# Performance work log

Hardware: AMD Instinct MI355X
Metric: run time of the kernel (lower is better)

## Reference

```python
import jax, jax.numpy as jnp
import numpy as np

N, P, C, K = 1024, 64, 64, 16
C_MID, C_OUT = 128, 128


def setup_inputs() -> dict:
    key = jax.random.key(0)
    k1, k2, k3, k4 = jax.random.split(key, 4)
    x = jax.random.normal(k1, (N, P, C), dtype=jnp.float32)
    mask = jnp.zeros((N, P), dtype=bool)  # True = padded particle
    # Conv2d(2C -> C_MID, 1x1, no bias); Conv2d(C_MID -> C_OUT, 1x1, no bias)
    W1 = jax.random.normal(k2, (C_MID, 2 * C), dtype=jnp.float32) * 0.05
    W2 = jax.random.normal(k3, (C_OUT, C_MID), dtype=jnp.float32) * 0.05
    # Conv1d(C -> C_OUT, kernel 1, no bias) residual path
    Wres = jax.random.normal(k4, (C_OUT, C), dtype=jnp.float32) * 0.05
    return {"x": x, "mask": mask, "W1": W1, "W2": W2, "Wres": Wres}


def reference(x, mask, W1, W2, Wres):
    n, p, c = x.shape
    k = K
    # residual: Conv1d kernel-1 == per-particle matmul  (N,P,C)->(N,P,C_OUT)
    x_res = jnp.einsum('npc,oc->npo', x, Wres)
    # direction = x with padded rows set to +inf (mask all False here)
    direction = jnp.where(mask[..., None], jnp.inf, x)
    # pairwise L2 distance over channel dim: (N,P,P)
    diff = direction[:, :, None, :] - direction[:, None, :, :]
    dist = jnp.sqrt(jnp.sum(diff * diff, axis=-1))
    # smallest K+1 distances, drop self
    _, idx = jax.lax.top_k(-dist, k + 1)
    knn = idx[..., 1:]  # (N,P,K)
    # faithful to torch: gather along the CHANNEL dim with particle indices
    f_center = jnp.broadcast_to(x[:, :, None, :], (n, p, k, c))  # (N,P,K,C)
    f_neighbor = jnp.take_along_axis(f_center, knn[..., None], axis=-1)  # (N,P,K,1)
    feat = jnp.concatenate([f_center, f_center - f_neighbor], axis=-1)  # (N,P,K,2C)
    # 1x1 conv MLP (channels-last layout)
    h = jax.nn.relu(jnp.einsum('npkc,oc->npko', feat, W1))
    h = jax.nn.relu(jnp.einsum('npkc,oc->npko', h, W2))  # (N,P,K,C_OUT)
    # mask neighbors pointing at padded slots, masked mean over K
    n_valid = p - jnp.sum(mask, axis=-1)  # (N,)
    mask_K = knn >= n_valid[:, None, None]  # (N,P,K) bool
    h = jnp.where(mask_K[..., None], 0.0, h)
    denom = (k - jnp.sum(mask_K, axis=-1)).astype(h.dtype)  # (N,P)
    agg = jnp.sum(h, axis=2) / denom[..., None]  # (N,P,C_OUT)
    return jax.nn.relu(agg + x_res)
```

## Files before the change

### kernel.cpp

```cpp
#include <hip/hip_runtime.h>
#include <hip/hip_bf16.h>

typedef __bf16 bf16x8 __attribute__((ext_vector_type(8)));
typedef float  f32x4  __attribute__((ext_vector_type(4)));
typedef float  f32x2  __attribute__((ext_vector_type(2)));
typedef unsigned long long u64;

#define MFMA_BF16 __builtin_amdgcn_mfma_f32_16x16x32_bf16

#define WS_W2P  (1u << 20)
#define WS_WCP  ((1u << 20) + 32768u)
#define WS_SSUM ((1u << 20) + 65536u)

#define K1_XS   0
#define K1_SD   17408
#define K1_SQ   34048
#define K1_LDS  38144

__global__ __launch_bounds__(256, 3)
void knn_kernel(const float* __restrict__ x, const float* __restrict__ W1,
                const float* __restrict__ W2, const float* __restrict__ Wres,
                unsigned* __restrict__ ws)
{
    __shared__ char smem[K1_LDS];
    float*    xs   = (float*)(smem + K1_XS);
    float*    D    = (float*)(smem + K1_SD);
    float*    sd_t = (float*)(smem + K1_SD);
    unsigned* sqp  = (unsigned*)(smem + K1_SQ);

    const int tid = threadIdx.x;
    const int n   = blockIdx.x;
    const float* __restrict__ xn = x + (size_t)n * 4096;

    #pragma unroll
    for (int i = 0; i < 4; ++i) {
        int e4 = tid + 256 * i;
        f32x4 v = *(const f32x4*)(xn + e4 * 4);
        int row = e4 >> 4, col = (e4 & 15) * 4;
        float* dst = xs + row * 68 + col;
        dst[0] = v[0]; dst[1] = v[1]; dst[2] = v[2]; dst[3] = v[3];
    }
    __syncthreads();

    {
#pragma clang fp contract(off)
        const int p = tid >> 2, rb = tid & 3;
        f32x4 xp4[16];
        const f32x4* xprow = (const f32x4*)(xs + p * 68);
        #pragma unroll
        for (int v = 0; v < 16; ++v) xp4[v] = xprow[v];

        const int d0 = (rb - p) & 3;
        #pragma unroll
        for (int t = 0; t < 8; ++t) {
            int delta = (d0 == 0) ? (4 + 4 * t) : (d0 + 4 * t);
            int q = (p + delta) & 63;
            bool doit = !(delta == 32 && p >= 32);
            if (doit) {
                const f32x4* xq4 = (const f32x4*)(xs + q * 68);
                f32x4 e0 = xp4[0] - xq4[0];
                f32x4 e1 = xp4[1] - xq4[1];
                f32x4 rA = e0 * e0;
                f32x4 rB = e1 * e1;
                #pragma unroll
                for (int b = 1; b < 8; ++b) {
                    f32x4 g0 = xp4[2*b]   - xq4[2*b];   rA = rA + g0 * g0;
                    f32x4 g1 = xp4[2*b+1] - xq4[2*b+1]; rB = rB + g1 * g1;
                }
                float d2 = ((rA[0]+rA[1]) + (rA[2]+rA[3])) + ((rB[0]+rB[1]) + (rB[2]+rB[3]));
                D[p * 65 + q] = d2;
                D[q * 65 + p] = d2;
            }
        }
        __syncthreads();

        u64 keys[16];
        #pragma unroll
        for (int i = 0; i < 16; ++i) {
            int q = 4 * i + rb;
            float d2  = D[p * 65 + q];
            float key = sqrtf(d2);
            unsigned kb = __float_as_uint(key);
            if (q == p) kb = 0x7f800000u;
            keys[i] = ((u64)kb << 8) | (unsigned)q;
        }
        __syncthreads();

        #pragma unroll
        for (int pp = 1; pp < 16; pp <<= 1) {
            #pragma unroll
            for (int k = pp; k >= 1; k >>= 1) {
                #pragma unroll
                for (int j = k & (pp - 1); j + k < 16; j += 2 * k) {
                    #pragma unroll
                    for (int i = 0; i < k; ++i) {
                        if (i + j + k < 16 && ((i + j) / (2 * pp) == (i + j + k) / (2 * pp))) {
                            u64 a = keys[i + j], b = keys[i + j + k];
                            u64 lo = a < b ? a : b;
                            u64 hi = a < b ? b : a;
                            keys[i + j] = lo; keys[i + j + k] = hi;
                        }
                    }
                }
            }
        }
        #pragma unroll
        for (int t = 0; t < 4; ++t) {
            unsigned wq = 0;
            #pragma unroll
            for (int b = 0; b < 4; ++b) {
                int s = 4 * t + b;
                sd_t[(rb * 16 + s) * 65 + p] = __uint_as_float((unsigned)(keys[s] >> 8));
                wq |= ((unsigned)(keys[s] & 0x3fu)) << (8 * b);
            }
            sqp[(rb * 4 + t) * 64 + p] = wq;
        }
    }
    __syncthreads();

    if (tid < 64) {
        const int p = tid;
        float dh[4]; unsigned qh[4]; int ix[4];
        #pragma unroll
        for (int b = 0; b < 4; ++b) {
            ix[b] = 0;
            dh[b] = sd_t[(b * 16) * 65 + p];
            qh[b] = sqp[(b * 4) * 64 + p] & 63u;
        }
        unsigned knacc[4] = {0u, 0u, 0u, 0u};
        for (int s = 0; s < 16; ++s) {
            int bsel = 0; float bd = dh[0]; unsigned bq = qh[0];
            #pragma unroll
            for (int b = 1; b < 4; ++b) {
                bool t = (dh[b] < bd) || (dh[b] == bd && qh[b] < bq);
                if (t) { bd = dh[b]; bq = qh[b]; bsel = b; }
            }
            knacc[s >> 2] |= bq << ((s & 3) * 8);
            int ni = ix[bsel] + 1; ix[bsel] = ni;
            int nc = ni < 15 ? ni : 15;
            float nd = sd_t[(bsel * 16 + nc) * 65 + p];
            unsigned nw = sqp[(bsel * 4 + (nc >> 2)) * 64 + p];
            unsigned nq = (nw >> ((nc & 3) * 8)) & 63u;
            if (ni > 15) nd = __builtin_inff();
            dh[bsel] = nd; qh[bsel] = nq;
        }
        *(uint4*)(ws + (size_t)n * 256 + p * 4) =
            make_uint4(knacc[0], knacc[1], knacc[2], knacc[3]);
    }

    if (n < 32) {
        if (tid < 64) {
            const int l = tid, f = n;
            int ntl = f >> 2, kt = f & 3;
            int o = ntl * 16 + (l & 15);
            int c = kt * 32 + (l >> 4) * 8;
            const float* s0 = W2 + o * 128 + c;
            f32x4 a0 = *(const f32x4*)s0, a1 = *(const f32x4*)(s0 + 4);
            bf16x8 fr;
            fr[0]=(__bf16)a0[0]; fr[1]=(__bf16)a0[1]; fr[2]=(__bf16)a0[2]; fr[3]=(__bf16)a0[3];
            fr[4]=(__bf16)a1[0]; fr[5]=(__bf16)a1[1]; fr[6]=(__bf16)a1[2]; fr[7]=(__bf16)a1[3];
            *(bf16x8*)((__bf16*)((char*)ws + WS_W2P) + (size_t)(f * 64 + l) * 8) = fr;
        }
    } else if (n < 64) {
        if (tid < 64) {
            const int l = tid, f = n - 32;
            int wv = f >> 3, rem = f & 7, ntl = rem >> 1, kt = rem & 1;
            int o = wv * 64 + ntl * 16 + (l & 15);
            int c = kt * 32 + (l >> 4) * 8;
            float v[8];
            if (o < 128) {
                const float* s0 = W1 + o * 128 + c;
                f32x4 a0 = *(const f32x4*)s0,      a1 = *(const f32x4*)(s0 + 4);
                f32x4 b0 = *(const f32x4*)(s0+64), b1 = *(const f32x4*)(s0 + 68);
                v[0]=a0[0]+b0[0]; v[1]=a0[1]+b0[1]; v[2]=a0[2]+b0[2]; v[3]=a0[3]+b0[3];
                v[4]=a1[0]+b1[0]; v[5]=a1[1]+b1[1]; v[6]=a1[2]+b1[2]; v[7]=a1[3]+b1[3];
            } else {
                const float* s0 = Wres + (o - 128) * 64 + c;
                f32x4 a0 = *(const f32x4*)s0, a1 = *(const f32x4*)(s0 + 4);
                v[0]=a0[0]; v[1]=a0[1]; v[2]=a0[2]; v[3]=a0[3];
                v[4]=a1[0]; v[5]=a1[1]; v[6]=a1[2]; v[7]=a1[3];
            }
            bf16x8 fr;
            #pragma unroll
            for (int j = 0; j < 8; ++j) fr[j] = (__bf16)v[j];
            *(bf16x8*)((__bf16*)((char*)ws + WS_WCP) + (size_t)(f * 64 + l) * 8) = fr;
        }
    } else if (n == 64) {
        if (tid < 128) {
            const f32x4* src = (const f32x4*)(W1 + tid * 128 + 64);
            f32x4 a = {0.f, 0.f, 0.f, 0.f};
            #pragma unroll
            for (int i = 0; i < 16; ++i) a += src[i];
            ((float*)((char*)ws + WS_SSUM))[tid] = a[0] + a[1] + a[2] + a[3];
        }
    }
}

#define K2_UB   0
#define K2_XR   32768
#define K2_SS   65536
#define K2_LDS  66048

__global__ __launch_bounds__(256, 2)
void gemm_kernel(const float* __restrict__ x, const unsigned* __restrict__ ws,
                 float* __restrict__ out)
{
    __shared__ char smem[K2_LDS];
    __bf16*   ub   = (__bf16*)(smem + K2_UB);
    __bf16*   xres = (__bf16*)(smem + K2_XR);
    float*    Ssum = (float*)(smem + K2_SS);

    const __bf16* __restrict__ w2p   = (const __bf16*)((const char*)ws + WS_W2P);
    const __bf16* __restrict__ wcp   = (const __bf16*)((const char*)ws + WS_WCP);
    const float*  __restrict__ ssums = (const float*)((const char*)ws + WS_SSUM);

    const int tid  = threadIdx.x;
    const int lane = tid & 63;
    const int w    = tid >> 6;
    const int lm   = lane & 15;
    const int lq   = lane >> 4;
    const int n0   = blockIdx.x * 2;

    if (tid < 128) Ssum[tid] = ssums[tid];

    {
        bf16x8 wcf[4][2];
        #pragma unroll
        for (int ntl = 0; ntl < 4; ++ntl) {
            #pragma unroll
            for (int kt = 0; kt < 2; ++kt)
                wcf[ntl][kt] = *(const bf16x8*)(wcp + (size_t)((w * 8 + ntl * 2 + kt) * 64 + lane) * 8);
        }
        #pragma unroll
        for (int ns = 0; ns < 2; ++ns) {
            const float* xn = x + (size_t)(n0 + ns) * 4096;
            __bf16* ubn = ub   + ns * 8192;
            __bf16* xrn = xres + ns * 8192;
            #pragma unroll
            for (int mt = 0; mt < 4; ++mt) {
                bf16x8 af[2];
                #pragma unroll
                for (int kt = 0; kt < 2; ++kt) {
                    const float* arow = xn + (mt * 16 + lm) * 64 + kt * 32 + lq * 8;
                    f32x4 a0 = *(const f32x4*)arow, a1 = *(const f32x4*)(arow + 4);
                    bf16x8 f;
                    f[0]=(__bf16)a0[0]; f[1]=(__bf16)a0[1]; f[2]=(__bf16)a0[2]; f[3]=(__bf16)a0[3];
                    f[4]=(__bf16)a1[0]; f[5]=(__bf16)a1[1]; f[6]=(__bf16)a1[2]; f[7]=(__bf16)a1[3];
                    af[kt] = f;
                }
                #pragma unroll
                for (int ntl = 0; ntl < 4; ++ntl) {
                    f32x4 acc = {0.f, 0.f, 0.f, 0.f};
                    acc = MFMA_BF16(af[0], wcf[ntl][0], acc, 0, 0, 0);
                    acc = MFMA_BF16(af[1], wcf[ntl][1], acc, 0, 0, 0);
                    int o = w * 64 + ntl * 16 + lm;
                    #pragma unroll
                    for (int r = 0; r < 4; ++r) {
                        int p = mt * 16 + lq * 4 + r;
                        if (o < 128) ubn[p * 128 + o] = (__bf16)acc[r];
                        else         xrn[p * 128 + (o - 128)] = (__bf16)acc[r];
                    }
                }
            }
        }
    }
    __syncthreads();

    {
        bf16x8 w2f[8][4];
        #pragma unroll
        for (int ntl = 0; ntl < 8; ++ntl) {
            #pragma unroll
            for (int kt = 0; kt < 4; ++kt)
                w2f[ntl][kt] = *(const bf16x8*)(w2p + (size_t)((ntl * 4 + kt) * 64 + lane) * 8);
        }
        f32x2 ss2[4][4];
        #pragma unroll
        for (int kt = 0; kt < 4; ++kt) {
            #pragma unroll
            for (int h = 0; h < 4; ++h) {
                ss2[kt][h][0] = Ssum[kt * 32 + lq * 8 + 2 * h];
                ss2[kt][h][1] = Ssum[kt * 32 + lq * 8 + 2 * h + 1];
            }
        }
        const int c0 = lq * 32 + lm;
        const int jsh = (lm & 3) * 8, jwi = lm >> 2;

        #pragma unroll 1
        for (int ns = 0; ns < 2; ++ns) {
            const float*    xn  = x + (size_t)(n0 + ns) * 4096;
            const unsigned* kb  = ws + (size_t)(n0 + ns) * 256;
            const __bf16*   ubn = ub   + ns * 8192;
            const __bf16*   xrn = xres + ns * 8192;
            const size_t outbase = (size_t)(n0 + ns) * 8192;

            unsigned jw_a = kb[w * 4 + jwi];
            unsigned jw_b = kb[(w + 4) * 4 + jwi];
            float sv_next = xn[w * 64 + ((jw_a >> jsh) & 63u)];

            #pragma unroll 1
            for (int pi = 0; pi < 16; ++pi) {
                const int p = w + pi * 4;
                const float sv_p = sv_next;
                jw_a = jw_b;
                if (pi < 15) {
                    if (pi < 14) jw_b = kb[(w + (pi + 2) * 4) * 4 + jwi];
                    sv_next = xn[(p + 4) * 64 + ((jw_a >> jsh) & 63u)];
                }

                const f32x2 sv2 = {sv_p, sv_p};
                f32x4 acc[8];
                #pragma unroll
                for (int ntl = 0; ntl < 8; ++ntl) acc[ntl] = f32x4{0.f, 0.f, 0.f, 0.f};
                #pragma unroll
                for (int kt = 0; kt < 4; ++kt) {
                    bf16x8 upv = *(const bf16x8*)(ubn + p * 128 + kt * 32 + lq * 8);
                    bf16x8 af;
                    #pragma unroll
                    for (int h = 0; h < 4; ++h) {
                        f32x2 u2 = { (float)upv[2*h], (float)upv[2*h+1] };
                        f32x2 m2 = u2 - sv2 * ss2[kt][h];
                        af[2*h]   = (__bf16)fmaxf(m2[0], 0.0f);
                        af[2*h+1] = (__bf16)fmaxf(m2[1], 0.0f);
                    }
                    #pragma unroll
                    for (int ntl = 0; ntl < 8; ++ntl)
                        acc[ntl] = MFMA_BF16(af, w2f[ntl][kt], acc[ntl], 0, 0, 0);
                }
                float part[8];
                #pragma unroll
                for (int ntl = 0; ntl < 8; ++ntl) {
                    part[ntl] = fmaxf(acc[ntl][0], 0.f) + fmaxf(acc[ntl][1], 0.f)
                              + fmaxf(acc[ntl][2], 0.f) + fmaxf(acc[ntl][3], 0.f);
                }
                float s1[4];
                #pragma unroll
                for (int i = 0; i < 4; ++i) {
                    float mine = (lq < 2) ? part[i] : part[4 + i];
                    float thr  = (lq < 2) ? part[4 + i] : part[i];
                    s1[i] = mine + __shfl_xor(thr, 32);
                }
                float r0, r1;
                {
                    float m0 = ((lq & 1) == 0) ? s1[0] : s1[2];
                    float m1 = ((lq & 1) == 0) ? s1[1] : s1[3];
                    float t0 = ((lq & 1) == 0) ? s1[2] : s1[0];
                    float t1 = ((lq & 1) == 0) ? s1[3] : s1[1];
                    r0 = m0 + __shfl_xor(t0, 16);
                    r1 = m1 + __shfl_xor(t1, 16);
                }
                float x0 = (float)xrn[p * 128 + c0];
                float x1 = (float)xrn[p * 128 + c0 + 16];
                out[outbase + p * 128 + c0]      = fmaxf(r0 * 0.0625f + x0, 0.0f);
                out[outbase + p * 128 + c0 + 16] = fmaxf(r1 * 0.0625f + x1, 0.0f);
            }
        }
    }
}

extern "C" void kernel_launch(void* const* d_in, const int* in_sizes, int n_in,
                              void* d_out, int out_size, void* d_ws, size_t ws_size,
                              hipStream_t stream) {
    const float* x    = (const float*)d_in[0];
    const float* W1   = (const float*)d_in[2];
    const float* W2   = (const float*)d_in[3];
    const float* Wres = (const float*)d_in[4];
    float* outp = (float*)d_out;
    unsigned* ws = (unsigned*)d_ws;
    int nblocks = in_sizes[0] / 4096;
    hipLaunchKernelGGL(knn_kernel,  dim3(nblocks), dim3(256), 0, stream,
                       x, W1, W2, Wres, ws);
    hipLaunchKernelGGL(gemm_kernel, dim3(nblocks / 2), dim3(256), 0, stream,
                       x, ws, outp);
}
```

Measured before the change: 151.8 us.

## Stage W2 in LDS, spill residual to output, and interleave two samples

The W2 fragments move from 128 VGPRs per lane into shared memory, taking over the LDS space that used to hold the bf16 residual. The residual is now written in fp32 straight into the output buffer and read back, with a threadfence before the barrier. The per-particle loop processes both samples of the block together, so each W2 fragment loaded from LDS feeds two MFMAs and there are two independent accumulator chains. The aim is to cut register pressure and add ILP, at the cost of extra LDS reads per MFMA pair and an extra global round trip for the residual.

```diff
diff --git a/kernel.cpp b/kernel.cpp
--- a/kernel.cpp
+++ b/kernel.cpp
@@ -196,8 +196,8 @@
     }
 }
 
-#define K2_UB   0
-#define K2_XR   32768
+#define K2_W2   0
+#define K2_UB   32768
 #define K2_SS   65536
 #define K2_LDS  66048
 
@@ -206,9 +206,9 @@
                  float* __restrict__ out)
 {
     __shared__ char smem[K2_LDS];
-    __bf16*   ub   = (__bf16*)(smem + K2_UB);
-    __bf16*   xres = (__bf16*)(smem + K2_XR);
-    float*    Ssum = (float*)(smem + K2_SS);
+    __bf16* w2l  = (__bf16*)(smem + K2_W2);
+    __bf16* ub   = (__bf16*)(smem + K2_UB);
+    float*  Ssum = (float*)(smem + K2_SS);
 
     const __bf16* __restrict__ w2p   = (const __bf16*)((const char*)ws + WS_W2P);
     const __bf16* __restrict__ wcp   = (const __bf16*)((const char*)ws + WS_WCP);
@@ -221,6 +221,11 @@
     const int lq   = lane >> 4;
     const int n0   = blockIdx.x * 2;
 
+    #pragma unroll
+    for (int i = 0; i < 8; ++i) {
+        int slot = tid + 256 * i;
+        *(bf16x8*)(w2l + (size_t)slot * 8) = *(const bf16x8*)(w2p + (size_t)slot * 8);
+    }
     if (tid < 128) Ssum[tid] = ssums[tid];
 
     {
@@ -234,8 +239,8 @@
         #pragma unroll
         for (int ns = 0; ns < 2; ++ns) {
             const float* xn = x + (size_t)(n0 + ns) * 4096;
-            __bf16* ubn = ub   + ns * 8192;
-            __bf16* xrn = xres + ns * 8192;
+            __bf16* ubn = ub + ns * 8192;
+            float*  on  = out + (size_t)(n0 + ns) * 8192;
             #pragma unroll
             for (int mt = 0; mt < 4; ++mt) {
                 bf16x8 af[2];
@@ -258,22 +263,16 @@
                     for (int r = 0; r < 4; ++r) {
                         int p = mt * 16 + lq * 4 + r;
                         if (o < 128) ubn[p * 128 + o] = (__bf16)acc[r];
-                        else         xrn[p * 128 + (o - 128)] = (__bf16)acc[r];
+                        else         on[p * 128 + (o - 128)] = acc[r];
                     }
                 }
             }
         }
     }
+    __threadfence();
     __syncthreads();
 
     {
-        bf16x8 w2f[8][4];
-        #pragma unroll
-        for (int ntl = 0; ntl < 8; ++ntl) {
-            #pragma unroll
-            for (int kt = 0; kt < 4; ++kt)
-                w2f[ntl][kt] = *(const bf16x8*)(w2p + (size_t)((ntl * 4 + kt) * 64 + lane) * 8);
-        }
         f32x2 ss2[4][4];
         #pragma unroll
         for (int kt = 0; kt < 4; ++kt) {
@@ -285,75 +284,100 @@
         }
         const int c0 = lq * 32 + lm;
         const int jsh = (lm & 3) * 8, jwi = lm >> 2;
+        const float*    xn0 = x + (size_t)n0 * 4096;
+        const float*    xn1 = xn0 + 4096;
+        const unsigned* kb0 = ws + (size_t)n0 * 256;
+        const unsigned* kb1 = kb0 + 256;
+        const __bf16*   ub0 = ub;
+        const __bf16*   ub1 = ub + 8192;
+        float* o0 = out + (size_t)n0 * 8192;
+        float* o1 = o0 + 8192;
+
+        float sva_n  = xn0[w * 64 + ((kb0[w * 4 + jwi] >> jsh) & 63u)];
+        float svb_n  = xn1[w * 64 + ((kb1[w * 4 + jwi] >> jsh) & 63u)];
+        float xra0_n = o0[w * 128 + c0], xra1_n = o0[w * 128 + c0 + 16];
+        float xrb0_n = o1[w * 128 + c0], xrb1_n = o1[w * 128 + c0 + 16];
 
         #pragma unroll 1
-        for (int ns = 0; ns < 2; ++ns) {
-            const float*    xn  = x + (size_t)(n0 + ns) * 4096;
-            const unsigned* kb  = ws + (size_t)(n0 + ns) * 256;
-            const __bf16*   ubn = ub   + ns * 8192;
-            const __bf16*   xrn = xres + ns * 8192;
-            const size_t outbase = (size_t)(n0 + ns) * 8192;
-
-            unsigned jw_a = kb[w * 4 + jwi];
-            unsigned jw_b = kb[(w + 4) * 4 + jwi];
-            float sv_next = xn[w * 64 + ((jw_a >> jsh) & 63u)];
-
-            #pragma unroll 1
-            for (int pi = 0; pi < 16; ++pi) {
-                const int p = w + pi * 4;
-                const float sv_p = sv_next;
-                jw_a = jw_b;
-                if (pi < 15) {
-                    if (pi < 14) jw_b = kb[(w + (pi + 2) * 4) * 4 + jwi];
-                    sv_next = xn[(p + 4) * 64 + ((jw_a >> jsh) & 63u)];
-                }
-
-                const f32x2 sv2 = {sv_p, sv_p};
-                f32x4 acc[8];
-                #pragma unroll
-                for (int ntl = 0; ntl < 8; ++ntl) acc[ntl] = f32x4{0.f, 0.f, 0.f, 0.f};
-                #pragma unroll
-                for (int kt = 0; kt < 4; ++kt) {
-                    bf16x8 upv = *(const bf16x8*)(ubn + p * 128 + kt * 32 + lq * 8);
-                    bf16x8 af;
-                    #pragma unroll
-                    for (int h = 0; h < 4; ++h) {
-                        f32x2 u2 = { (float)upv[2*h], (float)upv[2*h+1] };
-                        f32x2 m2 = u2 - sv2 * ss2[kt][h];
-                        af[2*h]   = (__bf16)fmaxf(m2[0], 0.0f);
-                        af[2*h+1] = (__bf16)fmaxf(m2[1], 0.0f);
-                    }
-                    #pragma unroll
-                    for (int ntl = 0; ntl < 8; ++ntl)
-                        acc[ntl] = MFMA_BF16(af, w2f[ntl][kt], acc[ntl], 0, 0, 0);
-                }
-                float part[8];
+        for (int pi = 0; pi < 16; ++pi) {
+            const int p = w + pi * 4;
+            const float sva = sva_n, svb = svb_n;
+            const float xra0 = xra0_n, xra1 = xra1_n;
+            const float xrb0 = xrb0_n, xrb1 = xrb1_n;
+            if (pi < 15) {
+                const int pn = p + 4;
+                sva_n  = xn0[pn * 64 + ((kb0[pn * 4 + jwi] >> jsh) & 63u)];
+                svb_n  = xn1[pn * 64 + ((kb1[pn * 4 + jwi] >> jsh) & 63u)];
+                xra0_n = o0[pn * 128 + c0]; xra1_n = o0[pn * 128 + c0 + 16];
+                xrb0_n = o1[pn * 128 + c0]; xrb1_n = o1[pn * 128 + c0 + 16];
+            }
+            bf16x8 afa[4], afb[4];
+            const f32x2 sa2 = {sva, sva}, sb2 = {svb, svb};
+            #pragma unroll
+            for (int kt = 0; kt < 4; ++kt) {
+                bf16x8 ua  = *(const bf16x8*)(ub0 + p * 128 + kt * 32 + lq * 8);
+                bf16x8 ubv = *(const bf16x8*)(ub1 + p * 128 + kt * 32 + lq * 8);
+                #pragma unroll
+                for (int h = 0; h < 4; ++h) {
+                    f32x2 u2a = { (float)ua[2*h],  (float)ua[2*h+1] };
+                    f32x2 m2a = u2a - sa2 * ss2[kt][h];
+                    afa[kt][2*h]   = (__bf16)fmaxf(m2a[0], 0.0f);
+                    afa[kt][2*h+1] = (__bf16)fmaxf(m2a[1], 0.0f);
+                    f32x2 u2b = { (float)ubv[2*h], (float)ubv[2*h+1] };
+                    f32x2 m2b = u2b - sb2 * ss2[kt][h];
+                    afb[kt][2*h]   = (__bf16)fmaxf(m2b[0], 0.0f);
+                    afb[kt][2*h+1] = (__bf16)fmaxf(m2b[1], 0.0f);
+                }
+            }
+            f32x4 acca[8], accb[8];
+            #pragma unroll
+            for (int ntl = 0; ntl < 8; ++ntl) {
+                acca[ntl] = f32x4{0.f, 0.f, 0.f, 0.f};
+                accb[ntl] = f32x4{0.f, 0.f, 0.f, 0.f};
+            }
+            #pragma unroll
+            for (int kt = 0; kt < 4; ++kt) {
                 #pragma unroll
                 for (int ntl = 0; ntl < 8; ++ntl) {
-                    part[ntl] = fmaxf(acc[ntl][0], 0.f) + fmaxf(acc[ntl][1], 0.f)
-                              + fmaxf(acc[ntl][2], 0.f) + fmaxf(acc[ntl][3], 0.f);
-                }
-                float s1[4];
-                #pragma unroll
-                for (int i = 0; i < 4; ++i) {
-                    float mine = (lq < 2) ? part[i] : part[4 + i];
-                    float thr  = (lq < 2) ? part[4 + i] : part[i];
-                    s1[i] = mine + __shfl_xor(thr, 32);
-                }
-                float r0, r1;
-                {
-                    float m0 = ((lq & 1) == 0) ? s1[0] : s1[2];
-                    float m1 = ((lq & 1) == 0) ? s1[1] : s1[3];
-                    float t0 = ((lq & 1) == 0) ? s1[2] : s1[0];
-                    float t1 = ((lq & 1) == 0) ? s1[3] : s1[1];
-                    r0 = m0 + __shfl_xor(t0, 16);
-                    r1 = m1 + __shfl_xor(t1, 16);
-                }
-                float x0 = (float)xrn[p * 128 + c0];
-                float x1 = (float)xrn[p * 128 + c0 + 16];
-                out[outbase + p * 128 + c0]      = fmaxf(r0 * 0.0625f + x0, 0.0f);
-                out[outbase + p * 128 + c0 + 16] = fmaxf(r1 * 0.0625f + x1, 0.0f);
-            }
+                    bf16x8 bf = *(const bf16x8*)(w2l + (size_t)((ntl * 4 + kt) * 64 + lane) * 8);
+                    acca[ntl] = MFMA_BF16(afa[kt], bf, acca[ntl], 0, 0, 0);
+                    accb[ntl] = MFMA_BF16(afb[kt], bf, accb[ntl], 0, 0, 0);
+                }
+            }
+            float parta[8], partb[8];
+            #pragma unroll
+            for (int ntl = 0; ntl < 8; ++ntl) {
+                parta[ntl] = fmaxf(acca[ntl][0], 0.f) + fmaxf(acca[ntl][1], 0.f)
+                           + fmaxf(acca[ntl][2], 0.f) + fmaxf(acca[ntl][3], 0.f);
+                partb[ntl] = fmaxf(accb[ntl][0], 0.f) + fmaxf(accb[ntl][1], 0.f)
+                           + fmaxf(accb[ntl][2], 0.f) + fmaxf(accb[ntl][3], 0.f);
+            }
+            float s1a[4], s1b[4];
+            #pragma unroll
+            for (int i = 0; i < 4; ++i) {
+                float ma = (lq < 2) ? parta[i] : parta[4 + i];
+                float ta = (lq < 2) ? parta[4 + i] : parta[i];
+                s1a[i] = ma + __shfl_xor(ta, 32);
+                float mb = (lq < 2) ? partb[i] : partb[4 + i];
+                float tb = (lq < 2) ? partb[4 + i] : partb[i];
+                s1b[i] = mb + __shfl_xor(tb, 32);
+            }
+            float r0a, r1a, r0b, r1b;
+            {
+                bool e = ((lq & 1) == 0);
+                float m0 = e ? s1a[0] : s1a[2], m1 = e ? s1a[1] : s1a[3];
+                float t0 = e ? s1a[2] : s1a[0], t1 = e ? s1a[3] : s1a[1];
+                r0a = m0 + __shfl_xor(t0, 16);
+                r1a = m1 + __shfl_xor(t1, 16);
+                float n0_ = e ? s1b[0] : s1b[2], n1_ = e ? s1b[1] : s1b[3];
+                float u0 = e ? s1b[2] : s1b[0], u1 = e ? s1b[3] : s1b[1];
+                r0b = n0_ + __shfl_xor(u0, 16);
+                r1b = n1_ + __shfl_xor(u1, 16);
+            }
+            o0[p * 128 + c0]      = fmaxf(r0a * 0.0625f + xra0, 0.0f);
+            o0[p * 128 + c0 + 16] = fmaxf(r1a * 0.0625f + xra1, 0.0f);
+            o1[p * 128 + c0]      = fmaxf(r0b * 0.0625f + xrb0, 0.0f);
+            o1[p * 128 + c0 + 16] = fmaxf(r1b * 0.0625f + xrb1, 0.0f);
         }
     }
 }
```

Result: slower. 214.6 us (+41.4%).
